# Kernel tuning notes

Hardware: AMD Instinct MI355X
Metric: run time of the kernel (lower is better)

The kernel has to match this reference:

```python
import jax, jax.numpy as jnp
import numpy as np

HEADS = 4
NEG_SLOPE_ATT = 0.2   # GATConv default negative_slope
NEG_SLOPE_ACT = 0.01  # torch.nn.LeakyReLU default


def setup_inputs() -> dict:
    key = jax.random.key(0)
    ks = jax.random.split(key, 10)
    N, F_IN, C, NCLS, B = 100000, 128, 32, 10, 128
    E = 1600000
    x = jax.random.normal(ks[0], (N, F_IN), dtype=jnp.float32)
    edge_index = jax.random.randint(ks[1], (2, E), 0, N, dtype=jnp.int64)
    batch = jnp.sort(jax.random.randint(ks[2], (N,), 0, B, dtype=jnp.int64))
    # GATConv parameters (eval mode: dropout inactive)
    W = jax.random.normal(ks[3], (F_IN, HEADS * C), dtype=jnp.float32) / np.sqrt(F_IN)
    att_src = jax.random.normal(ks[4], (HEADS, C), dtype=jnp.float32) / np.sqrt(C)
    att_dst = jax.random.normal(ks[5], (HEADS, C), dtype=jnp.float32) / np.sqrt(C)
    bias = jnp.zeros((HEADS * C,), dtype=jnp.float32)
    lin_w = jax.random.normal(ks[6], (NCLS, HEADS * C), dtype=jnp.float32) / np.sqrt(HEADS * C)
    lin_b = jnp.zeros((NCLS,), dtype=jnp.float32)
    return {"x": x, "edge_index": edge_index, "batch": batch, "batch_size": B,
            "W": W, "att_src": att_src, "att_dst": att_dst, "bias": bias,
            "lin_w": lin_w, "lin_b": lin_b}


def _leaky(v, s):
    return jnp.where(v >= 0, v, s * v)


def reference(x, edge_index, batch, batch_size, W, att_src, att_dst, bias, lin_w, lin_b):
    N = x.shape[0]
    H, C = att_src.shape
    xh = (x @ W).reshape(N, H, C)                      # [N,H,C]
    # add self-loops (GATConv default add_self_loops=True)
    loops = jnp.arange(N, dtype=edge_index.dtype)
    src = jnp.concatenate([edge_index[0], loops])      # [E+N]
    dst = jnp.concatenate([edge_index[1], loops])
    a_src = jnp.einsum('nhc,hc->nh', xh, att_src)      # [N,H]
    a_dst = jnp.einsum('nhc,hc->nh', xh, att_dst)
    e = _leaky(a_src[src] + a_dst[dst], NEG_SLOPE_ATT) # [E+N,H]
    # segment softmax over incoming edges of each dst node
    m = jax.ops.segment_max(e, dst, num_segments=N)
    e = jnp.exp(e - m[dst])
    s = jax.ops.segment_sum(e, dst, num_segments=N)
    alpha = e / (s[dst] + 1e-16)                       # [E+N,H]
    msg = xh[src] * alpha[..., None]                   # [E+N,H,C]
    out = jax.ops.segment_sum(msg, dst, num_segments=N).reshape(N, H * C) + bias
    out = _leaky(out, NEG_SLOPE_ACT)
    # global mean pool per graph
    summed = jax.ops.segment_sum(out, batch, num_segments=batch_size)
    counts = jax.ops.segment_sum(jnp.ones((N,), dtype=out.dtype), batch, num_segments=batch_size)
    pooled = summed / jnp.maximum(counts, 1.0)[:, None]
    return pooled @ lin_w.T + lin_b
```

## Files before the change

### kernel.cpp

```cpp
#include <hip/hip_runtime.h>
#include <hip/hip_fp16.h>

#define HC 128
#define FIN 128
#define NHEAD 4
#define NS_ATT 0.2f
#define NS_ACT 0.01f
#define NBLK_P 256
#define BCAP 14336

typedef _Float16 half8 __attribute__((ext_vector_type(8)));
typedef float f32x4 __attribute__((ext_vector_type(4)));

__device__ __forceinline__ float lrelu(float v, float s) { return v >= 0.f ? v : s * v; }

__device__ __forceinline__ int lowerb(const int* __restrict__ a, int n, int v) {
  int lo = 0, hi = n;
  while (lo < hi) {
    int m = (lo + hi) >> 1;
    if (a[m] < v) lo = m + 1; else hi = m;
  }
  return lo;
}

__global__ void k_init(float* __restrict__ pool_sum, int* __restrict__ pool_cnt, int B) {
  int i = blockIdx.x * 256 + threadIdx.x;
  if (i < B * HC) pool_sum[i] = 0.f;
  if (i < B) pool_cnt[i] = 0;
}

__global__ void k_wprep(const float* __restrict__ W, const float* __restrict__ att_s,
                        const float* __restrict__ att_d, _Float16* __restrict__ Wh) {
  const int nt = blockIdx.x, t = threadIdx.x;
  const int kt = t >> 6, l = t & 63;
  const int c = nt * 16 + (l & 15);
  const int kbase = kt * 32 + (l >> 4) * 8;
  half8 v8;
#pragma unroll
  for (int j = 0; j < 8; ++j) {
    const int k = kbase + j;
    float v = 0.f;
    if (c < 128) {
      v = W[k * HC + c];
    } else if (c < 132) {
      const int h = c - 128;
      for (int cc = 0; cc < 32; ++cc) v += W[k * HC + h * 32 + cc] * att_s[h * 32 + cc];
    } else if (c < 136) {
      const int h = c - 132;
      for (int cc = 0; cc < 32; ++cc) v += W[k * HC + h * 32 + cc] * att_d[h * 32 + cc];
    }
    v8[j] = (_Float16)v;
  }
  ((half8*)Wh)[(nt * 4 + kt) * 64 + l] = v8;
}

__global__ __launch_bounds__(256) void k_xw(
    const float* __restrict__ x, const _Float16* __restrict__ Wh,
    _Float16* __restrict__ xh, float* __restrict__ a_src, float* __restrict__ a_dst,
    int N) {
  const int wv = threadIdx.x >> 6, l = threadIdx.x & 63;
  const int r0 = blockIdx.x * 64 + wv * 16;
  if (r0 >= N) return;
  const int row_a = r0 + (l & 15);
  const long arow = (long)min(row_a, N - 1) * FIN;
  const int kg = (l >> 4) * 8;
  half8 afr[4];
#pragma unroll
  for (int kt = 0; kt < 4; ++kt) {
    const float4 p0 = *(const float4*)(x + arow + kt * 32 + kg);
    const float4 p1 = *(const float4*)(x + arow + kt * 32 + kg + 4);
    afr[kt][0] = (_Float16)p0.x; afr[kt][1] = (_Float16)p0.y;
    afr[kt][2] = (_Float16)p0.z; afr[kt][3] = (_Float16)p0.w;
    afr[kt][4] = (_Float16)p1.x; afr[kt][5] = (_Float16)p1.y;
    afr[kt][6] = (_Float16)p1.z; afr[kt][7] = (_Float16)p1.w;
  }
  const half8* __restrict__ Wh8 = (const half8*)Wh;
  const int rbase = r0 + (l >> 4) * 4;
  const int cc = l & 15;
#pragma unroll
  for (int nt = 0; nt < 9; ++nt) {
    half8 b0 = Wh8[(nt * 4 + 0) * 64 + l];
    half8 b1 = Wh8[(nt * 4 + 1) * 64 + l];
    half8 b2 = Wh8[(nt * 4 + 2) * 64 + l];
    half8 b3 = Wh8[(nt * 4 + 3) * 64 + l];
    f32x4 acc = {0.f, 0.f, 0.f, 0.f};
    acc = __builtin_amdgcn_mfma_f32_16x16x32_f16(afr[0], b0, acc, 0, 0, 0);
    acc = __builtin_amdgcn_mfma_f32_16x16x32_f16(afr[1], b1, acc, 0, 0, 0);
    acc = __builtin_amdgcn_mfma_f32_16x16x32_f16(afr[2], b2, acc, 0, 0, 0);
    acc = __builtin_amdgcn_mfma_f32_16x16x32_f16(afr[3], b3, acc, 0, 0, 0);
    if (nt < 8) {
      const int col = nt * 16 + cc;
#pragma unroll
      for (int r = 0; r < 4; ++r) {
        const int row = rbase + r;
        if (row < N) xh[(long)row * HC + col] = (_Float16)acc[r];
      }
    } else if (cc < 8) {
      float* __restrict__ dst = (cc < 4) ? a_src : a_dst;
      const int h = cc & 3;
#pragma unroll
      for (int r = 0; r < 4; ++r) {
        const int row = rbase + r;
        if (row < N) dst[row * NHEAD + h] = acc[r];
      }
    }
  }
}

__global__ __launch_bounds__(256) void k_hist(const int* __restrict__ ei,
                                              int* __restrict__ hist, int E, int NBUCK, int CH) {
  __shared__ int lc[512];
  for (int i = threadIdx.x; i < NBUCK; i += 256) lc[i] = 0;
  __syncthreads();
  const int e0 = blockIdx.x * CH, e1 = min(E, e0 + CH);
  for (int e = e0 + threadIdx.x; e < e1; e += 256) {
    atomicAdd(&lc[ei[E + e] >> 9], 1);
  }
  __syncthreads();
  for (int i = threadIdx.x; i < NBUCK; i += 256) hist[i * gridDim.x + blockIdx.x] = lc[i];
}

__global__ void k_scanA(const int* __restrict__ cnt, int* __restrict__ offs,
                        int* __restrict__ part, int N) {
  __shared__ int s[256];
  int t = threadIdx.x, i = blockIdx.x * 256 + t;
  int v = (i < N) ? cnt[i] : 0;
  s[t] = v;
#pragma unroll
  for (int off = 1; off < 256; off <<= 1) {
    __syncthreads();
    int u = (t >= off) ? s[t - off] : 0;
    __syncthreads();
    s[t] += u;
  }
  if (i < N) offs[i] = s[t] - v;
  if (t == 255) part[blockIdx.x] = s[255];
}

__global__ void k_scanB(int* __restrict__ part, int NB) {
  __shared__ int s[1024];
  int t = threadIdx.x;
  int v = (t < NB) ? part[t] : 0;
  s[t] = v;
#pragma unroll
  for (int off = 1; off < 1024; off <<= 1) {
    __syncthreads();
    int u = (t >= off) ? s[t - off] : 0;
    __syncthreads();
    s[t] += u;
  }
  if (t < NB) part[t] = s[t] - v;
  if (t == 1023) part[NB] = s[1023];
}

__global__ void k_scanC(int* __restrict__ offs, const int* __restrict__ part, int N, int NB) {
  int i = blockIdx.x * 256 + threadIdx.x;
  if (i < N) offs[i] += part[i >> 8];
  else if (i == N) offs[N] = part[NB];
}

__global__ __launch_bounds__(256) void k_part(const int* __restrict__ ei,
                                              const int* __restrict__ histoffs,
                                              unsigned* __restrict__ ebuf,
                                              int E, int NBUCK, int CH) {
  __shared__ int lcur[512];
  for (int i = threadIdx.x; i < NBUCK; i += 256)
    lcur[i] = histoffs[i * gridDim.x + blockIdx.x];
  __syncthreads();
  const int e0 = blockIdx.x * CH, e1 = min(E, e0 + CH);
  for (int e = e0 + threadIdx.x; e < e1; e += 256) {
    const int s = ei[e], d = ei[E + e];
    const int pos = atomicAdd(&lcur[d >> 9], 1);
    ebuf[pos] = ((unsigned)(d & 511) << 18) | (unsigned)s;
  }
}

__global__ __launch_bounds__(256) void k_build(
    const int* __restrict__ histoffs, const unsigned* __restrict__ ebuf,
    int* __restrict__ csr_src, int* __restrict__ offs, int N) {
  const int b = blockIdx.x, t = threadIdx.x;
  const int n0 = b << 9, n1 = min(N, n0 + 512), nn = n1 - n0;
  const int eb0 = histoffs[b * NBLK_P];
  const int eb1 = histoffs[(b + 1) * NBLK_P];
  const int base = eb0 + n0;
  const int L = (eb1 - eb0) + nn;
  __shared__ int cnt2[512];
  __shared__ int scn[256];
  __shared__ int cur[512];
  __shared__ int lcsr[BCAP];
  cnt2[t] = 0; cnt2[t + 256] = 0;
  __syncthreads();
  for (int e = eb0 + t; e < eb1; e += 256) atomicAdd(&cnt2[ebuf[e] >> 18], 1);
  __syncthreads();
  const int i0 = 2 * t, i1 = 2 * t + 1;
  const int a0 = (i0 < nn) ? cnt2[i0] + 1 : 0;
  const int a1 = (i1 < nn) ? cnt2[i1] + 1 : 0;
  scn[t] = a0 + a1;
  for (int off = 1; off < 256; off <<= 1) {
    __syncthreads();
    int u = (t >= off) ? scn[t - off] : 0;
    __syncthreads();
    scn[t] += u;
  }
  __syncthreads();
  const int ex = scn[t] - (a0 + a1);
  const int o0 = ex, o1 = ex + a0;
  if (i0 < nn) offs[n0 + i0] = base + o0;
  if (i1 < nn) offs[n0 + i1] = base + o1;
  if (t == 255 && n1 == N) offs[N] = base + scn[255];
  if (L <= BCAP) {
    if (i0 < nn) { lcsr[o0] = n0 + i0; cur[i0] = o0 + 1; }
    if (i1 < nn) { lcsr[o1] = n0 + i1; cur[i1] = o1 + 1; }
    __syncthreads();
    for (int e = eb0 + t; e < eb1; e += 256) {
      const unsigned pk = ebuf[e];
      const int pos = atomicAdd(&cur[pk >> 18], 1);
      lcsr[pos] = (int)(pk & 0x3FFFFu);
    }
    __syncthreads();
    for (int i = t; i < L; i += 256) csr_src[base + i] = lcsr[i];
  } else {
    if (i0 < nn) { csr_src[base + o0] = n0 + i0; cur[i0] = base + o0 + 1; }
    if (i1 < nn) { csr_src[base + o1] = n0 + i1; cur[i1] = base + o1 + 1; }
    __syncthreads();
    for (int e = eb0 + t; e < eb1; e += 256) {
      const unsigned pk = ebuf[e];
      const int pos = atomicAdd(&cur[pk >> 18], 1);
      csr_src[pos] = (int)(pk & 0x3FFFFu);
    }
  }
}

__global__ __launch_bounds__(256) void k_agg(
    const int* __restrict__ csr_src, const int* __restrict__ offs,
    const float* __restrict__ a_src, const float* __restrict__ a_dst,
    const __half* __restrict__ xh, const float* __restrict__ bias,
    __half* __restrict__ xout, int N) {
  __shared__ float wls[4][64 * 5];
  __shared__ int sls[4][64];
  const int wv = threadIdx.x >> 6;
  const int wid = (blockIdx.x * 256 + threadIdx.x) >> 6;
  const int lane = threadIdx.x & 63;
  if (wid >= N) return;
  float* __restrict__ wl = wls[wv];
  int* __restrict__ sl = sls[wv];
  const int n = wid;
  const int o0 = offs[n], deg = offs[n + 1] - o0;
  const float4 dv = ((const float4*)a_dst)[n];
  const int l16 = lane & 15, g = lane >> 4, h = l16 >> 2;
  const uint4* __restrict__ xh16 = (const uint4*)xh;

  float4 sm = make_float4(0.f, 0.f, 0.f, 0.f);
  float acc[8] = {0.f, 0.f, 0.f, 0.f, 0.f, 0.f, 0.f, 0.f};

  for (int c0 = 0; c0 < deg; c0 += 64) {
    const int cl = min(64, deg - c0);
    if (lane < cl) {
      const int sj = csr_src[o0 + c0 + lane];
      const float4 av = ((const float4*)a_src)[sj];
      const float w0 = __expf(lrelu(av.x + dv.x, NS_ATT));
      const float w1 = __expf(lrelu(av.y + dv.y, NS_ATT));
      const float w2 = __expf(lrelu(av.z + dv.z, NS_ATT));
      const float w3 = __expf(lrelu(av.w + dv.w, NS_ATT));
      sm.x += w0; sm.y += w1; sm.z += w2; sm.w += w3;
      sl[lane] = sj;
      wl[lane * 5 + 0] = w0; wl[lane * 5 + 1] = w1;
      wl[lane * 5 + 2] = w2; wl[lane * 5 + 3] = w3;
    }
    for (int j = 0; j < cl; j += 16) {
      int s[4];
      float wsel[4];
      uint4 u[4];
#pragma unroll
      for (int q = 0; q < 4; ++q) {
        const int ee = j + q * 4 + g;
        const bool valid = ee < cl;
        const float wv_ = wl[ee * 5 + h];
        const int ss = sl[ee];
        wsel[q] = valid ? wv_ : 0.f;
        s[q] = valid ? ss : 0;
      }
#pragma unroll
      for (int q = 0; q < 4; ++q) {
        u[q] = xh16[(long)s[q] * 16 + l16];
      }
#pragma unroll
      for (int q = 0; q < 4; ++q) {
        const __half2* hp = (const __half2*)&u[q];
        const float2 f0 = __half22float2(hp[0]);
        const float2 f1 = __half22float2(hp[1]);
        const float2 f2 = __half22float2(hp[2]);
        const float2 f3 = __half22float2(hp[3]);
        acc[0] = fmaf(wsel[q], f0.x, acc[0]); acc[1] = fmaf(wsel[q], f0.y, acc[1]);
        acc[2] = fmaf(wsel[q], f1.x, acc[2]); acc[3] = fmaf(wsel[q], f1.y, acc[3]);
        acc[4] = fmaf(wsel[q], f2.x, acc[4]); acc[5] = fmaf(wsel[q], f2.y, acc[5]);
        acc[6] = fmaf(wsel[q], f3.x, acc[6]); acc[7] = fmaf(wsel[q], f3.y, acc[7]);
      }
    }
  }

#pragma unroll
  for (int m = 32; m >= 1; m >>= 1) {
    sm.x += __shfl_xor(sm.x, m);
    sm.y += __shfl_xor(sm.y, m);
    sm.z += __shfl_xor(sm.z, m);
    sm.w += __shfl_xor(sm.w, m);
  }
#pragma unroll
  for (int m = 32; m >= 16; m >>= 1) {
#pragma unroll
    for (int i = 0; i < 8; ++i) acc[i] += __shfl_xor(acc[i], m);
  }

  const float sh = (h == 0) ? sm.x : (h == 1) ? sm.y : (h == 2) ? sm.z : sm.w;
  const float inv = 1.f / (sh + 1e-16f);
  const int ch = l16 * 8 + g * 2;
  float r0 = lrelu(acc[2 * g] * inv + bias[ch], NS_ACT);
  float r1 = lrelu(acc[2 * g + 1] * inv + bias[ch + 1], NS_ACT);
  ((__half2*)(xout + (long)n * HC))[ch >> 1] = __floats2half2_rn(r0, r1);
}

__global__ __launch_bounds__(256) void k_pool(
    const __half* __restrict__ xout, const int* __restrict__ batch,
    float* __restrict__ pool_sum, int* __restrict__ pool_cnt, int N) {
  const int b = blockIdx.x, q = blockIdx.y, t = threadIdx.x;
  const int lo = lowerb(batch, N, b);
  const int hi = lowerb(batch, N, b + 1);
  const int cnt = hi - lo;
  if (q == 0 && t == 0) pool_cnt[b] = cnt;
  const int qlen = (cnt + 3) >> 2;
  const int qlo = lo + q * qlen;
  const int qhi = min(qlo + qlen, hi);

  const int c2 = t & 63;
  const int rs = t >> 6;
  const __half2* __restrict__ xo2 = (const __half2*)xout;
  float ax = 0.f, ay = 0.f, bx2 = 0.f, by2 = 0.f;
  int r = qlo + rs;
  for (; r + 4 < qhi; r += 8) {
    float2 f0 = __half22float2(xo2[(long)r * 64 + c2]);
    float2 f1 = __half22float2(xo2[(long)(r + 4) * 64 + c2]);
    ax += f0.x; ay += f0.y; bx2 += f1.x; by2 += f1.y;
  }
  for (; r < qhi; r += 4) {
    float2 f0 = __half22float2(xo2[(long)r * 64 + c2]);
    ax += f0.x; ay += f0.y;
  }
  __shared__ float2 sp[256];
  sp[t] = make_float2(ax + bx2, ay + by2);
  __syncthreads();
  if (t < 64) {
    float2 s0 = sp[t], s1 = sp[t + 64], s2 = sp[t + 128], s3 = sp[t + 192];
    atomicAdd(&pool_sum[b * HC + 2 * t], (s0.x + s1.x) + (s2.x + s3.x));
    atomicAdd(&pool_sum[b * HC + 2 * t + 1], (s0.y + s1.y) + (s2.y + s3.y));
  }
}

__global__ void k_final(const float* __restrict__ pool_sum, const int* __restrict__ pool_cnt,
                        const float* __restrict__ lin_w, const float* __restrict__ lin_b,
                        float* __restrict__ out, int B) {
  int b = blockIdx.x;
  __shared__ float pl[HC];
  int t = threadIdx.x;
  float c = fmaxf((float)pool_cnt[b], 1.0f);
  pl[t] = pool_sum[b * HC + t] / c;
  __syncthreads();
  if (t < 10) {
    float a = lin_b[t];
    for (int k = 0; k < HC; ++k) a = fmaf(pl[k], lin_w[t * HC + k], a);
    out[b * 10 + t] = a;
  }
}

extern "C" void kernel_launch(void* const* d_in, const int* in_sizes, int n_in,
                              void* d_out, int out_size, void* d_ws, size_t ws_size,
                              hipStream_t stream) {
  const float* x = (const float*)d_in[0];
  const int* ei = (const int*)d_in[1];
  const int* batch = (const int*)d_in[2];
  const float* Wm = (const float*)d_in[4];
  const float* att_s = (const float*)d_in[5];
  const float* att_d = (const float*)d_in[6];
  const float* bias = (const float*)d_in[7];
  const float* lin_w = (const float*)d_in[8];
  const float* lin_b = (const float*)d_in[9];
  float* out = (float*)d_out;

  const int N = in_sizes[2];
  const int E = in_sizes[1] / 2;
  const int B = out_size / 10;
  const int NBUCK = (N + 511) >> 9;
  const int M = NBUCK * NBLK_P;
  const int NB2 = (M + 255) / 256;
  const int CH = (E + NBLK_P - 1) / NBLK_P;

  char* p = (char*)d_ws;
  auto carve = [&](size_t bytes) {
    void* r = (void*)p;
    p += (bytes + 255) & ~(size_t)255;
    return r;
  };
  __half* xh = (__half*)carve((size_t)N * HC * 2);
  __half* xout = (__half*)carve((size_t)N * HC * 2);
  float* a_src = (float*)carve((size_t)N * NHEAD * 4);
  float* a_dst = (float*)carve((size_t)N * NHEAD * 4);
  int* offs = (int*)carve((size_t)(N + 1) * 4);
  int* csr_src = (int*)carve((size_t)(N + (size_t)E) * 4);
  float* pool_sum = (float*)carve((size_t)B * HC * 4);
  int* pool_cnt = (int*)carve((size_t)B * 4);
  _Float16* Wh = (_Float16*)carve((size_t)9 * 4 * 64 * 8 * 2);

  char* q = (char*)xout;
  auto carve2 = [&](size_t bytes) {
    void* r = (void*)q;
    q += (bytes + 255) & ~(size_t)255;
    return r;
  };
  unsigned* ebuf = (unsigned*)carve2((size_t)E * 4);
  int* hist = (int*)carve2((size_t)M * 4);
  int* histoffs = (int*)carve2((size_t)(M + 1) * 4);
  int* part2 = (int*)carve2((size_t)(NB2 + 2) * 4);

  k_init<<<(B * HC + 255) / 256, 256, 0, stream>>>(pool_sum, pool_cnt, B);
  k_wprep<<<9, 256, 0, stream>>>(Wm, att_s, att_d, Wh);
  k_xw<<<(N + 63) / 64, 256, 0, stream>>>(x, Wh, (_Float16*)xh, a_src, a_dst, N);
  k_hist<<<NBLK_P, 256, 0, stream>>>(ei, hist, E, NBUCK, CH);
  k_scanA<<<NB2, 256, 0, stream>>>(hist, histoffs, part2, M);
  k_scanB<<<1, 1024, 0, stream>>>(part2, NB2);
  k_scanC<<<(M + 256) / 256, 256, 0, stream>>>(histoffs, part2, M, NB2);
  k_part<<<NBLK_P, 256, 0, stream>>>(ei, histoffs, ebuf, E, NBUCK, CH);
  k_build<<<NBUCK, 256, 0, stream>>>(histoffs, ebuf, csr_src, offs, N);
  k_agg<<<(N + 3) / 4, 256, 0, stream>>>(csr_src, offs, a_src, a_dst, xh, bias, xout, N);
  k_pool<<<dim3(B, 4), 256, 0, stream>>>(xout, batch, pool_sum, pool_cnt, N);
  k_final<<<B, 128, 0, stream>>>(pool_sum, pool_cnt, lin_w, lin_b, out, B);
}
```

Measured before the change: 190.2 us.

## Fuse small setup kernels, single-block scan, LDS-staged xh stores, fused pool+final

Merges the weight-prep and histogram kernels into one launch, and replaces the three-kernel scan with a single 1024-thread block scan. Stages the xh MFMA outputs through LDS so they go out as 16-byte row stores instead of scattered 2-byte stores. Merges pooling and the final linear layer into one kernel per graph, which removes the zero-init kernel and the atomics. This cuts launch count and uncoalesced writes, at the cost of less pooling parallelism (one block per graph instead of four) and a serial per-thread scan loop.

```diff
diff --git a/kernel.cpp b/kernel.cpp
--- a/kernel.cpp
+++ b/kernel.cpp
@@ -23,41 +23,50 @@
   return lo;
 }
 
-__global__ void k_init(float* __restrict__ pool_sum, int* __restrict__ pool_cnt, int B) {
-  int i = blockIdx.x * 256 + threadIdx.x;
-  if (i < B * HC) pool_sum[i] = 0.f;
-  if (i < B) pool_cnt[i] = 0;
-}
-
-__global__ void k_wprep(const float* __restrict__ W, const float* __restrict__ att_s,
-                        const float* __restrict__ att_d, _Float16* __restrict__ Wh) {
-  const int nt = blockIdx.x, t = threadIdx.x;
-  const int kt = t >> 6, l = t & 63;
-  const int c = nt * 16 + (l & 15);
-  const int kbase = kt * 32 + (l >> 4) * 8;
-  half8 v8;
-#pragma unroll
-  for (int j = 0; j < 8; ++j) {
-    const int k = kbase + j;
-    float v = 0.f;
-    if (c < 128) {
-      v = W[k * HC + c];
-    } else if (c < 132) {
-      const int h = c - 128;
-      for (int cc = 0; cc < 32; ++cc) v += W[k * HC + h * 32 + cc] * att_s[h * 32 + cc];
-    } else if (c < 136) {
-      const int h = c - 132;
-      for (int cc = 0; cc < 32; ++cc) v += W[k * HC + h * 32 + cc] * att_d[h * 32 + cc];
-    }
-    v8[j] = (_Float16)v;
-  }
-  ((half8*)Wh)[(nt * 4 + kt) * 64 + l] = v8;
+__global__ __launch_bounds__(256) void k_hw(
+    const int* __restrict__ ei, int* __restrict__ hist, int E, int NBUCK, int CH,
+    const float* __restrict__ W, const float* __restrict__ att_s,
+    const float* __restrict__ att_d, _Float16* __restrict__ Wh) {
+  if (blockIdx.x >= NBLK_P) {
+    const int nt = blockIdx.x - NBLK_P, t = threadIdx.x;
+    const int kt = t >> 6, l = t & 63;
+    const int c = nt * 16 + (l & 15);
+    const int kbase = kt * 32 + (l >> 4) * 8;
+    half8 v8;
+#pragma unroll
+    for (int j = 0; j < 8; ++j) {
+      const int k = kbase + j;
+      float v = 0.f;
+      if (c < 128) {
+        v = W[k * HC + c];
+      } else if (c < 132) {
+        const int h = c - 128;
+        for (int cc = 0; cc < 32; ++cc) v += W[k * HC + h * 32 + cc] * att_s[h * 32 + cc];
+      } else if (c < 136) {
+        const int h = c - 132;
+        for (int cc = 0; cc < 32; ++cc) v += W[k * HC + h * 32 + cc] * att_d[h * 32 + cc];
+      }
+      v8[j] = (_Float16)v;
+    }
+    ((half8*)Wh)[(nt * 4 + kt) * 64 + l] = v8;
+    return;
+  }
+  __shared__ int lc[512];
+  for (int i = threadIdx.x; i < NBUCK; i += 256) lc[i] = 0;
+  __syncthreads();
+  const int e0 = blockIdx.x * CH, e1 = min(E, e0 + CH);
+  for (int e = e0 + threadIdx.x; e < e1; e += 256) {
+    atomicAdd(&lc[ei[E + e] >> 9], 1);
+  }
+  __syncthreads();
+  for (int i = threadIdx.x; i < NBUCK; i += 256) hist[i * NBLK_P + blockIdx.x] = lc[i];
 }
 
 __global__ __launch_bounds__(256) void k_xw(
     const float* __restrict__ x, const _Float16* __restrict__ Wh,
     _Float16* __restrict__ xh, float* __restrict__ a_src, float* __restrict__ a_dst,
     int N) {
+  __shared__ _Float16 xs[4][16][HC + 8];
   const int wv = threadIdx.x >> 6, l = threadIdx.x & 63;
   const int r0 = blockIdx.x * 64 + wv * 16;
   if (r0 >= N) return;
@@ -75,7 +84,7 @@
     afr[kt][6] = (_Float16)p1.z; afr[kt][7] = (_Float16)p1.w;
   }
   const half8* __restrict__ Wh8 = (const half8*)Wh;
-  const int rbase = r0 + (l >> 4) * 4;
+  const int rloc = (l >> 4) * 4;
   const int cc = l & 15;
 #pragma unroll
   for (int nt = 0; nt < 9; ++nt) {
@@ -91,72 +100,51 @@
     if (nt < 8) {
       const int col = nt * 16 + cc;
 #pragma unroll
-      for (int r = 0; r < 4; ++r) {
-        const int row = rbase + r;
-        if (row < N) xh[(long)row * HC + col] = (_Float16)acc[r];
-      }
+      for (int r = 0; r < 4; ++r) xs[wv][rloc + r][col] = (_Float16)acc[r];
     } else if (cc < 8) {
       float* __restrict__ dst = (cc < 4) ? a_src : a_dst;
       const int h = cc & 3;
 #pragma unroll
       for (int r = 0; r < 4; ++r) {
-        const int row = rbase + r;
+        const int row = r0 + rloc + r;
         if (row < N) dst[row * NHEAD + h] = acc[r];
       }
     }
   }
-}
-
-__global__ __launch_bounds__(256) void k_hist(const int* __restrict__ ei,
-                                              int* __restrict__ hist, int E, int NBUCK, int CH) {
-  __shared__ int lc[512];
-  for (int i = threadIdx.x; i < NBUCK; i += 256) lc[i] = 0;
-  __syncthreads();
-  const int e0 = blockIdx.x * CH, e1 = min(E, e0 + CH);
-  for (int e = e0 + threadIdx.x; e < e1; e += 256) {
-    atomicAdd(&lc[ei[E + e] >> 9], 1);
-  }
-  __syncthreads();
-  for (int i = threadIdx.x; i < NBUCK; i += 256) hist[i * gridDim.x + blockIdx.x] = lc[i];
-}
-
-__global__ void k_scanA(const int* __restrict__ cnt, int* __restrict__ offs,
-                        int* __restrict__ part, int N) {
-  __shared__ int s[256];
-  int t = threadIdx.x, i = blockIdx.x * 256 + t;
-  int v = (i < N) ? cnt[i] : 0;
-  s[t] = v;
-#pragma unroll
-  for (int off = 1; off < 256; off <<= 1) {
+#pragma unroll
+  for (int i = 0; i < 4; ++i) {
+    const int lr = (l >> 4) + i * 4;
+    const int row = r0 + lr;
+    if (row < N) {
+      const uint4 v = *(const uint4*)&xs[wv][lr][(l & 15) * 8];
+      *(uint4*)(xh + (long)row * HC + (l & 15) * 8) = v;
+    }
+  }
+}
+
+__global__ __launch_bounds__(1024) void k_scan1(const int* __restrict__ data,
+                                                int* __restrict__ offs, int M) {
+  __shared__ int s[1024];
+  const int t = threadIdx.x;
+  const int CHK = (M + 1023) >> 10;
+  const int lo = t * CHK, hi = min(M, lo + CHK);
+  int sum = 0;
+  for (int i = lo; i < hi; ++i) sum += data[i];
+  s[t] = sum;
+  for (int off = 1; off < 1024; off <<= 1) {
     __syncthreads();
     int u = (t >= off) ? s[t - off] : 0;
     __syncthreads();
     s[t] += u;
   }
-  if (i < N) offs[i] = s[t] - v;
-  if (t == 255) part[blockIdx.x] = s[255];
-}
-
-__global__ void k_scanB(int* __restrict__ part, int NB) {
-  __shared__ int s[1024];
-  int t = threadIdx.x;
-  int v = (t < NB) ? part[t] : 0;
-  s[t] = v;
-#pragma unroll
-  for (int off = 1; off < 1024; off <<= 1) {
-    __syncthreads();
-    int u = (t >= off) ? s[t - off] : 0;
-    __syncthreads();
-    s[t] += u;
-  }
-  if (t < NB) part[t] = s[t] - v;
-  if (t == 1023) part[NB] = s[1023];
-}
-
-__global__ void k_scanC(int* __restrict__ offs, const int* __restrict__ part, int N, int NB) {
-  int i = blockIdx.x * 256 + threadIdx.x;
-  if (i < N) offs[i] += part[i >> 8];
-  else if (i == N) offs[N] = part[NB];
+  __syncthreads();
+  int pre = s[t] - sum;
+  for (int i = lo; i < hi; ++i) {
+    const int v = data[i];
+    offs[i] = pre;
+    pre += v;
+  }
+  if (t == 1023) offs[M] = s[1023];
 }
 
 __global__ __launch_bounds__(256) void k_part(const int* __restrict__ ei,
@@ -165,7 +153,7 @@
                                               int E, int NBUCK, int CH) {
   __shared__ int lcur[512];
   for (int i = threadIdx.x; i < NBUCK; i += 256)
-    lcur[i] = histoffs[i * gridDim.x + blockIdx.x];
+    lcur[i] = histoffs[i * NBLK_P + blockIdx.x];
   __syncthreads();
   const int e0 = blockIdx.x * CH, e1 = min(E, e0 + CH);
   for (int e = e0 + threadIdx.x; e < e1; e += 256) {
@@ -320,50 +308,38 @@
   ((__half2*)(xout + (long)n * HC))[ch >> 1] = __floats2half2_rn(r0, r1);
 }
 
-__global__ __launch_bounds__(256) void k_pool(
+__global__ __launch_bounds__(256) void k_poolfinal(
     const __half* __restrict__ xout, const int* __restrict__ batch,
-    float* __restrict__ pool_sum, int* __restrict__ pool_cnt, int N) {
-  const int b = blockIdx.x, q = blockIdx.y, t = threadIdx.x;
+    const float* __restrict__ lin_w, const float* __restrict__ lin_b,
+    float* __restrict__ out, int N, int B) {
+  const int b = blockIdx.x, t = threadIdx.x;
   const int lo = lowerb(batch, N, b);
   const int hi = lowerb(batch, N, b + 1);
   const int cnt = hi - lo;
-  if (q == 0 && t == 0) pool_cnt[b] = cnt;
-  const int qlen = (cnt + 3) >> 2;
-  const int qlo = lo + q * qlen;
-  const int qhi = min(qlo + qlen, hi);
-
   const int c2 = t & 63;
   const int rs = t >> 6;
   const __half2* __restrict__ xo2 = (const __half2*)xout;
   float ax = 0.f, ay = 0.f, bx2 = 0.f, by2 = 0.f;
-  int r = qlo + rs;
-  for (; r + 4 < qhi; r += 8) {
+  int r = lo + rs;
+  for (; r + 4 < hi; r += 8) {
     float2 f0 = __half22float2(xo2[(long)r * 64 + c2]);
     float2 f1 = __half22float2(xo2[(long)(r + 4) * 64 + c2]);
     ax += f0.x; ay += f0.y; bx2 += f1.x; by2 += f1.y;
   }
-  for (; r < qhi; r += 4) {
+  for (; r < hi; r += 4) {
     float2 f0 = __half22float2(xo2[(long)r * 64 + c2]);
     ax += f0.x; ay += f0.y;
   }
   __shared__ float2 sp[256];
+  __shared__ float pl[HC];
   sp[t] = make_float2(ax + bx2, ay + by2);
   __syncthreads();
   if (t < 64) {
     float2 s0 = sp[t], s1 = sp[t + 64], s2 = sp[t + 128], s3 = sp[t + 192];
-    atomicAdd(&pool_sum[b * HC + 2 * t], (s0.x + s1.x) + (s2.x + s3.x));
-    atomicAdd(&pool_sum[b * HC + 2 * t + 1], (s0.y + s1.y) + (s2.y + s3.y));
-  }
-}
-
-__global__ void k_final(const float* __restrict__ pool_sum, const int* __restrict__ pool_cnt,
-                        const float* __restrict__ lin_w, const float* __restrict__ lin_b,
-                        float* __restrict__ out, int B) {
-  int b = blockIdx.x;
-  __shared__ float pl[HC];
-  int t = threadIdx.x;
-  float c = fmaxf((float)pool_cnt[b], 1.0f);
-  pl[t] = pool_sum[b * HC + t] / c;
+    const float c = fmaxf((float)cnt, 1.0f);
+    pl[2 * t] = ((s0.x + s1.x) + (s2.x + s3.x)) / c;
+    pl[2 * t + 1] = ((s0.y + s1.y) + (s2.y + s3.y)) / c;
+  }
   __syncthreads();
   if (t < 10) {
     float a = lin_b[t];
@@ -391,7 +367,6 @@
   const int B = out_size / 10;
   const int NBUCK = (N + 511) >> 9;
   const int M = NBUCK * NBLK_P;
-  const int NB2 = (M + 255) / 256;
   const int CH = (E + NBLK_P - 1) / NBLK_P;
 
   char* p = (char*)d_ws;
@@ -406,8 +381,6 @@
   float* a_dst = (float*)carve((size_t)N * NHEAD * 4);
   int* offs = (int*)carve((size_t)(N + 1) * 4);
   int* csr_src = (int*)carve((size_t)(N + (size_t)E) * 4);
-  float* pool_sum = (float*)carve((size_t)B * HC * 4);
-  int* pool_cnt = (int*)carve((size_t)B * 4);
   _Float16* Wh = (_Float16*)carve((size_t)9 * 4 * 64 * 8 * 2);
 
   char* q = (char*)xout;
@@ -419,18 +392,12 @@
   unsigned* ebuf = (unsigned*)carve2((size_t)E * 4);
   int* hist = (int*)carve2((size_t)M * 4);
   int* histoffs = (int*)carve2((size_t)(M + 1) * 4);
-  int* part2 = (int*)carve2((size_t)(NB2 + 2) * 4);
-
-  k_init<<<(B * HC + 255) / 256, 256, 0, stream>>>(pool_sum, pool_cnt, B);
-  k_wprep<<<9, 256, 0, stream>>>(Wm, att_s, att_d, Wh);
+
+  k_hw<<<NBLK_P + 9, 256, 0, stream>>>(ei, hist, E, NBUCK, CH, Wm, att_s, att_d, Wh);
   k_xw<<<(N + 63) / 64, 256, 0, stream>>>(x, Wh, (_Float16*)xh, a_src, a_dst, N);
-  k_hist<<<NBLK_P, 256, 0, stream>>>(ei, hist, E, NBUCK, CH);
-  k_scanA<<<NB2, 256, 0, stream>>>(hist, histoffs, part2, M);
-  k_scanB<<<1, 1024, 0, stream>>>(part2, NB2);
-  k_scanC<<<(M + 256) / 256, 256, 0, stream>>>(histoffs, part2, M, NB2);
+  k_scan1<<<1, 1024, 0, stream>>>(hist, histoffs, M);
   k_part<<<NBLK_P, 256, 0, stream>>>(ei, histoffs, ebuf, E, NBUCK, CH);
   k_build<<<NBUCK, 256, 0, stream>>>(histoffs, ebuf, csr_src, offs, N);
   k_agg<<<(N + 3) / 4, 256, 0, stream>>>(csr_src, offs, a_src, a_dst, xh, bias, xout, N);
-  k_pool<<<dim3(B, 4), 256, 0, stream>>>(xout, batch, pool_sum, pool_cnt, N);
-  k_final<<<B, 128, 0, stream>>>(pool_sum, pool_cnt, lin_w, lin_b, out, B);
-}
+  k_poolfinal<<<B, 256, 0, stream>>>(xout, batch, lin_w, lin_b, out, N, B);
+}
```

Result: slower. 260.6 us (+37.0%).
